# Optimization experiments

Hardware: AMD Instinct MI355X
Metric: run time of the kernel (lower is better)

## Reference

```python
import jax, jax.numpy as jnp
import numpy as np
from jax import lax

B, DIM, H, W = 4, 128, 128, 128
HEADS = 8
HID = int(DIM * 2.66)  # 340, IEL hidden_features
EPS_LN = 1e-6


def conv(x, w, b=None, groups=1, pad=0):
    out = lax.conv_general_dilated(
        x, w, (1, 1), [(pad, pad), (pad, pad)],
        feature_group_count=groups,
        dimension_numbers=('NCHW', 'OIHW', 'NCHW'))
    if b is not None:
        out = out + b[None, :, None, None]
    return out


def setup_inputs() -> dict:
    key = jax.random.key(0)
    ks = jax.random.split(key, 16)
    def wgt(k, shape, s=0.05):
        return jax.random.normal(k, shape, jnp.float32) * s
    return dict(
        x=jax.random.normal(ks[0], (B, DIM, H, W), jnp.float32),
        y=jax.random.normal(ks[1], (B, DIM, H, W), jnp.float32),
        ln_w=jnp.ones((DIM,), jnp.float32),
        ln_b=jnp.zeros((DIM,), jnp.float32),
        temperature=jnp.ones((HEADS, 1, 1), jnp.float32),
        q_w=wgt(ks[2], (DIM, DIM, 1, 1)),
        qdw_w=wgt(ks[3], (DIM, 1, 3, 3)),
        kv_w=wgt(ks[4], (2 * DIM, DIM, 1, 1)),
        kvdw_w=wgt(ks[5], (2 * DIM, 1, 3, 3)),
        po_w=wgt(ks[6], (DIM, DIM, 1, 1)),
        g1_w=wgt(ks[7], (DIM // 2, DIM, 1, 1)),
        g1_b=jnp.zeros((DIM // 2,), jnp.float32),
        g2_w=wgt(ks[8], (1, DIM // 2, 1, 1)),
        g2_b=jnp.zeros((1,), jnp.float32),
        pin_w=wgt(ks[9], (2 * HID, DIM, 1, 1)),
        dw_w=wgt(ks[10], (2 * HID, 1, 3, 3)),
        dw1_w=wgt(ks[11], (HID, 1, 3, 3)),
        dw2_w=wgt(ks[12], (HID, 1, 3, 3)),
        pout_w=wgt(ks[13], (DIM, HID, 1, 1)),
    )


def reference(x, y, ln_w, ln_b, temperature, q_w, qdw_w, kv_w, kvdw_w, po_w,
              g1_w, g1_b, g2_w, g2_b, pin_w, dw_w, dw1_w, dw2_w, pout_w):
    Bn, C, Hh, Ww = x.shape
    ch = C // HEADS  # channel tokens per head

    def ln(z):  # channels_first LayerNorm over channel axis
        u = z.mean(1, keepdims=True)
        s = ((z - u) ** 2).mean(1, keepdims=True)
        return ln_w[None, :, None, None] * ((z - u) / jnp.sqrt(s + EPS_LN)) + ln_b[None, :, None, None]

    xn = ln(x)
    yn = ln(y)

    # SCAB: transposed (channel) attention with dynamic top-k mask
    q = conv(conv(xn, q_w), qdw_w, groups=C, pad=1)
    kv = conv(conv(yn, kv_w), kvdw_w, groups=2 * C, pad=1)
    k, v = jnp.split(kv, 2, axis=1)
    q = q.reshape(Bn, HEADS, ch, Hh * Ww)
    k = k.reshape(Bn, HEADS, ch, Hh * Ww)
    v = v.reshape(Bn, HEADS, ch, Hh * Ww)
    q = q / jnp.maximum(jnp.linalg.norm(q, axis=-1, keepdims=True), 1e-12)
    k = k / jnp.maximum(jnp.linalg.norm(k, axis=-1, keepdims=True), 1e-12)

    # gate -> dynamic_k = int(ch * mean(gate)) as in torch (truncation)
    g = jax.nn.sigmoid(conv(jax.nn.relu(conv(xn, g1_w, g1_b)), g2_w, g2_b))
    dk = jnp.clip((ch * lax.stop_gradient(g).mean()).astype(jnp.int32), 1, ch)

    attn = jnp.einsum('bhcn,bhdn->bhcd', q, k) * temperature[None]  # [B,H,ch,ch]
    order = jnp.argsort(-attn, axis=-1)       # topk ordering (descending)
    ranks = jnp.argsort(order, axis=-1)       # rank of each entry in its row
    attn = jnp.where(ranks < dk, attn, -jnp.inf)
    attn = jax.nn.softmax(attn, axis=-1)
    out = jnp.einsum('bhcd,bhdn->bhcn', attn, v).reshape(Bn, C, Hh, Ww)
    x = x + conv(out, po_w)

    # IEL: tanh-gated dwconv FFN
    z = ln(x)
    t = conv(conv(z, pin_w), dw_w, groups=2 * HID, pad=1)
    x1, x2 = jnp.split(t, 2, axis=1)
    x1 = jnp.tanh(conv(x1, dw1_w, groups=HID, pad=1)) + x1
    x2 = jnp.tanh(conv(x2, dw2_w, groups=HID, pad=1)) + x2
    return conv(x1 * x2, pout_w) + x
```

## Files before the change

### kernel.cpp

```cpp
#include <hip/hip_runtime.h>
#include <math.h>

static constexpr int Bn    = 4;
static constexpr int Cc    = 128;
static constexpr int Hh    = 128;
static constexpr int Wb    = 128;
static constexpr int Nn    = Hh * Wb;
static constexpr int HEADS = 8;
static constexpr int CHh   = 16;
static constexpr int HID   = 340;
static constexpr int HID2  = 680;
static constexpr int NS    = 64;
static constexpr int MPAD  = 704;
static constexpr int KPAD2 = 352;

typedef unsigned short ushort_t;
typedef __attribute__((ext_vector_type(8))) short short8;
typedef __attribute__((ext_vector_type(4))) float f32x4;

__device__ __forceinline__ ushort_t f2bf(float f) {
    unsigned u = __float_as_uint(f);
    return (ushort_t)((u + 0x7FFFu + ((u >> 16) & 1u)) >> 16);
}
__device__ __forceinline__ float bf2f(ushort_t h) {
    return __uint_as_float(((unsigned)h) << 16);
}

__device__ __forceinline__ float fast_tanh(float x) {
    float a = fabsf(x);
    a = fminf(a, 12.0f);
    float e = __expf(2.0f * a);
    float r = 1.0f - 2.0f * __builtin_amdgcn_rcpf(e + 1.0f);
    return x < 0.0f ? -r : r;
}

__device__ __forceinline__ void iel_stage(float (*ts)[136], const ushort_t* __restrict__ tp,
                                          int gy0, int tid) {
    for (int idx = tid; idx < 640; idx += 256) {
        int i  = idx >> 5;
        int ch = idx & 31;
        int gy = gy0 - 2 + i;
        float v0, v1, v2, v3;
        if (gy >= 0 && gy < Hh) {
            uint2 u = *(const uint2*)(tp + gy * Wb + ch * 4);
            v0 = bf2f((ushort_t)(u.x & 0xFFFF)); v1 = bf2f((ushort_t)(u.x >> 16));
            v2 = bf2f((ushort_t)(u.y & 0xFFFF)); v3 = bf2f((ushort_t)(u.y >> 16));
        } else {
            v0 = v1 = v2 = v3 = 0.f;
        }
        float* dst = &ts[i][2 + ch * 4];
        float2 w0; w0.x = v0; w0.y = v1;
        float2 w1; w1.x = v2; w1.y = v3;
        *(float2*)dst       = w0;
        *(float2*)(dst + 2) = w1;
        if (ch == 0)  { ts[i][0]   = 0.f; ts[i][1]   = 0.f; }
        if (ch == 31) { ts[i][130] = 0.f; ts[i][131] = 0.f; }
    }
}

__global__ __launch_bounds__(256) void ln_kernel(const float* __restrict__ in,
                                                 const float* __restrict__ w,
                                                 const float* __restrict__ bias,
                                                 float* __restrict__ out) {
    int p = blockIdx.x * 256 + threadIdx.x;
    int b = blockIdx.z;
    const float* ib = in + (size_t)b * Cc * Nn + p;
    float s = 0.f, s2 = 0.f;
    #pragma unroll 8
    for (int c = 0; c < Cc; ++c) {
        float v = ib[(size_t)c * Nn];
        s += v; s2 += v * v;
    }
    float mean = s * (1.0f / Cc);
    float var  = s2 * (1.0f / Cc) - mean * mean;
    float inv  = 1.0f / sqrtf(var + 1e-6f);
    float* ob = out + (size_t)b * Cc * Nn + p;
    #pragma unroll 8
    for (int c = 0; c < Cc; ++c) {
        float v = ib[(size_t)c * Nn];
        ob[(size_t)c * Nn] = w[c] * ((v - mean) * inv) + bias[c];
    }
}

__global__ __launch_bounds__(256) void ln_bf16_kernel(const float* __restrict__ in,
                                                      const float* __restrict__ w,
                                                      const float* __restrict__ bias,
                                                      ushort_t* __restrict__ out) {
    int p = blockIdx.x * 256 + threadIdx.x;
    int b = blockIdx.z;
    const float* ib = in + (size_t)b * Cc * Nn + p;
    float s = 0.f, s2 = 0.f;
    #pragma unroll 8
    for (int c = 0; c < Cc; ++c) {
        float v = ib[(size_t)c * Nn];
        s += v; s2 += v * v;
    }
    float mean = s * (1.0f / Cc);
    float var  = s2 * (1.0f / Cc) - mean * mean;
    float inv  = 1.0f / sqrtf(var + 1e-6f);
    ushort_t* ob = out + (size_t)b * Cc * Nn + p;
    #pragma unroll 8
    for (int c = 0; c < Cc; ++c) {
        float v = ib[(size_t)c * Nn];
        ob[(size_t)c * Nn] = f2bf(w[c] * ((v - mean) * inv) + bias[c]);
    }
}

__global__ __launch_bounds__(256) void wconv_pad_rows_kernel(const float* __restrict__ w,
                                                             ushort_t* __restrict__ o,
                                                             int rows, int K) {
    int idx = blockIdx.x * 256 + threadIdx.x;
    int r = idx / K, k = idx - r * K;
    o[idx] = (r < rows) ? f2bf(w[(size_t)r * K + k]) : (ushort_t)0;
}
__global__ __launch_bounds__(256) void wconv_pad_cols_kernel(const float* __restrict__ w,
                                                             ushort_t* __restrict__ o,
                                                             int K, int Kp) {
    int idx = blockIdx.x * 256 + threadIdx.x;
    int r = idx / Kp, k = idx - r * Kp;
    o[idx] = (k < K) ? f2bf(w[(size_t)r * K + k]) : (ushort_t)0;
}

__global__ __launch_bounds__(256) void zero_f32_kernel(float* __restrict__ p, int n) {
    int i = blockIdx.x * 256 + threadIdx.x;
    if (i < n) p[i] = 0.f;
}

__global__ __launch_bounds__(256) void compose_w5_kernel(const float* __restrict__ dww,
                                                         const float* __restrict__ dw1p,
                                                         const float* __restrict__ dw2p,
                                                         float* __restrict__ w5) {
    int idx = blockIdx.x * 256 + threadIdx.x;
    if (idx >= 2 * HID * 25) return;
    int t   = idx / (HID * 25);
    int rem = idx - t * HID * 25;
    int c   = rem / 25;
    int e   = rem - c * 25;
    int dy  = e / 5, dx = e - dy * 5;
    const float* wa = dww + ((size_t)t * HID + c) * 9;
    const float* wb = (t ? dw2p : dw1p) + (size_t)c * 9;
    float acc = 0.f;
    #pragma unroll
    for (int a = 0; a < 3; ++a)
        #pragma unroll
        for (int b2 = 0; b2 < 3; ++b2) {
            int cy = dy - a, cx = dx - b2;
            if (cy >= 0 && cy < 3 && cx >= 0 && cx < 3)
                acc += wb[a * 3 + b2] * wa[cy * 3 + cx];
        }
    w5[idx] = acc;
}

__global__ __launch_bounds__(256) void gemm_bf16_kernel(const ushort_t* __restrict__ Zh,
                                                        const ushort_t* __restrict__ Wh,
                                                        const float* __restrict__ bias,
                                                        const float* __restrict__ res,
                                                        float* outf,
                                                        ushort_t* outh,
                                                        int Cin, int Kpad, int Mreal,
                                                        int act) {
    const int b    = blockIdx.z;
    const int px0  = blockIdx.x * 128;
    const int co0  = blockIdx.y * 64;
    const int tid  = threadIdx.x;
    const int wv   = tid >> 6;
    const int lane = tid & 63;
    const int n    = lane & 15;
    const int q    = lane >> 4;

    __shared__ ushort_t Bl[128][40];

    const ushort_t* Zb = Zh + (size_t)b * Cin * Nn;

    f32x4 acc[4][2];
    #pragma unroll
    for (int i = 0; i < 4; ++i)
        #pragma unroll
        for (int j = 0; j < 2; ++j) acc[i][j] = (f32x4){0.f, 0.f, 0.f, 0.f};

    for (int k0 = 0; k0 < Kpad; k0 += 32) {
        {
            int r = tid >> 3;
            int s = tid & 7;
            int ci = k0 + r;
            ushort_t tmp[16];
            if (ci < Cin) {
                const ushort_t* src = Zb + (size_t)ci * Nn + px0 + s * 16;
                uint4 v0 = *(const uint4*)src;
                uint4 v1 = *(const uint4*)(src + 8);
                tmp[0]  = (ushort_t)(v0.x & 0xFFFF); tmp[1]  = (ushort_t)(v0.x >> 16);
                tmp[2]  = (ushort_t)(v0.y & 0xFFFF); tmp[3]  = (ushort_t)(v0.y >> 16);
                tmp[4]  = (ushort_t)(v0.z & 0xFFFF); tmp[5]  = (ushort_t)(v0.z >> 16);
                tmp[6]  = (ushort_t)(v0.w & 0xFFFF); tmp[7]  = (ushort_t)(v0.w >> 16);
                tmp[8]  = (ushort_t)(v1.x & 0xFFFF); tmp[9]  = (ushort_t)(v1.x >> 16);
                tmp[10] = (ushort_t)(v1.y & 0xFFFF); tmp[11] = (ushort_t)(v1.y >> 16);
                tmp[12] = (ushort_t)(v1.z & 0xFFFF); tmp[13] = (ushort_t)(v1.z >> 16);
                tmp[14] = (ushort_t)(v1.w & 0xFFFF); tmp[15] = (ushort_t)(v1.w >> 16);
            } else {
                #pragma unroll
                for (int i = 0; i < 16; ++i) tmp[i] = 0;
            }
            #pragma unroll
            for (int i = 0; i < 16; ++i) Bl[s * 16 + i][r] = tmp[i];
        }
        __syncthreads();

        short8 bfrag[2];
        #pragma unroll
        for (int px16 = 0; px16 < 2; ++px16)
            bfrag[px16] = *(const short8*)&Bl[wv * 32 + px16 * 16 + n][q * 8];
        #pragma unroll
        for (int mt = 0; mt < 4; ++mt) {
            const ushort_t* wp = Wh + (size_t)(co0 + mt * 16 + n) * Kpad + k0 + q * 8;
            short8 afrag = *(const short8*)wp;
            #pragma unroll
            for (int px16 = 0; px16 < 2; ++px16)
                acc[mt][px16] = __builtin_amdgcn_mfma_f32_16x16x32_bf16(
                    afrag, bfrag[px16], acc[mt][px16], 0, 0, 0);
        }
        __syncthreads();
    }

    #pragma unroll
    for (int px16 = 0; px16 < 2; ++px16) {
        int px = px0 + wv * 32 + px16 * 16 + n;
        #pragma unroll
        for (int mt = 0; mt < 4; ++mt) {
            #pragma unroll
            for (int reg = 0; reg < 4; ++reg) {
                int co = co0 + mt * 16 + q * 4 + reg;
                if (co < Mreal) {
                    float v = acc[mt][px16][reg];
                    if (bias) v += bias[co];
                    if (act == 1) v = fmaxf(v, 0.f);
                    size_t o = ((size_t)b * Mreal + co) * Nn + px;
                    if (res)  v += res[o];
                    if (outf) outf[o] = v;
                    if (outh) outh[o] = f2bf(v);
                }
            }
        }
    }
}

template <int TCO>
__global__ __launch_bounds__(256) void conv1x1v_kernel(const float* __restrict__ in,
                                                       const float* __restrict__ wgt,
                                                       int wstride,
                                                       const float* __restrict__ bias,
                                                       const float* __restrict__ res,
                                                       float* __restrict__ out,
                                                       int Cin, int Cout, int act) {
    int pg  = blockIdx.x * 256 + threadIdx.x;
    int b   = blockIdx.z;
    int co0 = blockIdx.y * TCO;

    const float* wrow[TCO];
    #pragma unroll
    for (int i = 0; i < TCO; ++i) {
        int co = co0 + i; if (co > Cout - 1) co = Cout - 1;
        wrow[i] = wgt + (size_t)co * wstride;
    }

    float4 acc[TCO];
    #pragma unroll
    for (int i = 0; i < TCO; ++i) acc[i] = make_float4(0.f, 0.f, 0.f, 0.f);

    const float* ib = in + (size_t)b * Cin * Nn + (size_t)pg * 4;
    #pragma unroll 8
    for (int ci = 0; ci < Cin; ++ci) {
        float4 v = *(const float4*)(ib + (size_t)ci * Nn);
        #pragma unroll
        for (int i = 0; i < TCO; ++i) {
            float w = wrow[i][ci];
            acc[i].x += v.x * w; acc[i].y += v.y * w;
            acc[i].z += v.z * w; acc[i].w += v.w * w;
        }
    }

    #pragma unroll
    for (int i = 0; i < TCO; ++i) {
        int co = co0 + i;
        if (co < Cout) {
            float4 r = acc[i];
            if (bias) { float bb = bias[co]; r.x += bb; r.y += bb; r.z += bb; r.w += bb; }
            if (act == 1) {
                r.x = fmaxf(r.x, 0.f); r.y = fmaxf(r.y, 0.f);
                r.z = fmaxf(r.z, 0.f); r.w = fmaxf(r.w, 0.f);
            }
            size_t o = ((size_t)b * Cout + co) * Nn + (size_t)pg * 4;
            if (res) {
                float4 rv = *(const float4*)(res + o);
                r.x += rv.x; r.y += rv.y; r.z += rv.z; r.w += rv.w;
            }
            *(float4*)(out + o) = r;
        }
    }
}

__global__ __launch_bounds__(256) void dw3x3_kernel(const float* __restrict__ in,
                                                    const float* __restrict__ w,
                                                    float* __restrict__ out, int Ct) {
    int p = blockIdx.x * 256 + threadIdx.x;
    int c = blockIdx.y;
    int b = blockIdx.z;
    int y = p >> 7, x = p & (Wb - 1);
    const float* ib = in + ((size_t)b * Ct + c) * Nn;
    float wl[9];
    #pragma unroll
    for (int k = 0; k < 9; ++k) wl[k] = w[c * 9 + k];
    float acc = 0.f;
    #pragma unroll
    for (int dy = 0; dy < 3; ++dy) {
        int yy = y + dy - 1;
        if (yy < 0 || yy >= Hh) continue;
        #pragma unroll
        for (int dx = 0; dx < 3; ++dx) {
            int xx = x + dx - 1;
            if (xx < 0 || xx >= Wb) continue;
            acc += wl[dy * 3 + dx] * ib[yy * Wb + xx];
        }
    }
    out[((size_t)b * Ct + c) * Nn + p] = acc;
}

__global__ __launch_bounds__(256) void dw3x3_bf16_v2_kernel(const ushort_t* __restrict__ in,
                                                            const float* __restrict__ w,
                                                            float* __restrict__ out, int Ct,
                                                            float* __restrict__ ssq,
                                                            int nrmC) {
    const int gy0 = blockIdx.x * 16;
    const int c   = blockIdx.y;
    const int b   = blockIdx.z;
    const int tid = threadIdx.x;

    __shared__ float ts[20][136];

    const ushort_t* ib = in + ((size_t)b * Ct + c) * Nn;
    iel_stage(ts, ib, gy0, tid);
    __syncthreads();

    float wl[9];
    #pragma unroll
    for (int k = 0; k < 9; ++k) wl[k] = w[c * 9 + k];

    float* ob = out + ((size_t)b * Ct + c) * Nn;
    float s2sum = 0.f;
    #pragma unroll
    for (int it = 0; it < 2; ++it) {
        int idx = tid + it * 256;
        int r  = idx >> 5;
        int x0 = (idx & 31) * 4;
        float a[4] = {0.f, 0.f, 0.f, 0.f};
        #pragma unroll
        for (int dy = 0; dy < 3; ++dy) {
            const float* row = &ts[r + 1 + dy][x0];
            float4 va = *(const float4*)row;
            float4 vb = *(const float4*)(row + 4);
            float e[8] = {va.x, va.y, va.z, va.w, vb.x, vb.y, vb.z, vb.w};
            const float* wr = wl + dy * 3;
            #pragma unroll
            for (int p = 0; p < 4; ++p)
                a[p] += wr[0] * e[p + 1] + wr[1] * e[p + 2] + wr[2] * e[p + 3];
        }
        float4 st; st.x = a[0]; st.y = a[1]; st.z = a[2]; st.w = a[3];
        *(float4*)(ob + (gy0 + r) * Wb + x0) = st;
        s2sum += a[0] * a[0] + a[1] * a[1] + a[2] * a[2] + a[3] * a[3];
    }

    if (ssq != nullptr && c < nrmC) {
        #pragma unroll
        for (int o = 32; o > 0; o >>= 1) s2sum += __shfl_xor(s2sum, o, 64);
        if ((tid & 63) == 0) atomicAdd(&ssq[(size_t)b * nrmC + c], s2sum);
    }
}

__global__ __launch_bounds__(256) void l2norm_kernel(float* __restrict__ data, int cstride) {
    int b = blockIdx.z, c = blockIdx.x;
    float* ptr = data + ((size_t)b * cstride + c) * Nn;
    int t = threadIdx.x;
    float s = 0.f;
    for (int i = t; i < Nn; i += 256) { float v = ptr[i]; s += v * v; }
    __shared__ float red[256];
    red[t] = s; __syncthreads();
    for (int st = 128; st > 0; st >>= 1) { if (t < st) red[t] += red[t + st]; __syncthreads(); }
    float scale = 1.0f / fmaxf(sqrtf(red[0]), 1e-12f);
    for (int i = t; i < Nn; i += 256) ptr[i] *= scale;
}

__global__ __launch_bounds__(256) void gate2_kernel(const float* __restrict__ gmid,
                                                    const float* __restrict__ w2,
                                                    const float* __restrict__ b2,
                                                    float* __restrict__ blocksums,
                                                    int out_off) {
    int p = blockIdx.x * 256 + threadIdx.x;
    int b = blockIdx.z;
    float acc = b2[0];
    const float* ib = gmid + (size_t)b * 64 * Nn + p;
    #pragma unroll 8
    for (int ci = 0; ci < 64; ++ci) acc += ib[(size_t)ci * Nn] * w2[ci];
    float g = 1.0f / (1.0f + expf(-acc));
    __shared__ float red[256];
    int t = threadIdx.x;
    red[t] = g; __syncthreads();
    for (int st = 128; st > 0; st >>= 1) { if (t < st) red[t] += red[t + st]; __syncthreads(); }
    if (t == 0) blocksums[out_off + b * 64 + blockIdx.x] = red[0];
}

__global__ void gate_final_kernel(const float* __restrict__ blocksums,
                                  int* __restrict__ dk_out) {
    __shared__ double sred[256];
    int t = threadIdx.x;
    sred[t] = (double)blocksums[t];
    __syncthreads();
    for (int st = 128; st > 0; st >>= 1) { if (t < st) sred[t] += sred[t + st]; __syncthreads(); }
    if (t == 0) {
        double mean = sred[0] / (double)(Bn * Nn);
        float val = 16.0f * (float)mean;
        int dk = (int)val;
        if (dk < 1) dk = 1;
        if (dk > 16) dk = 16;
        *dk_out = dk;
    }
}

__global__ __launch_bounds__(256) void attn_qk_partial_kernel(const float* __restrict__ q,
                                                              const float* __restrict__ k,
                                                              int kstride,
                                                              float* __restrict__ partial) {
    int ns = blockIdx.x, h = blockIdx.y, b = blockIdx.z;
    int t = threadIdx.x;
    int c = t >> 4, d = t & 15;
    __shared__ float qs[16][65];
    __shared__ float ks[16][65];
    const float* qb = q + ((size_t)b * Cc + h * CHh) * Nn;
    const float* kb = k + ((size_t)b * kstride + h * CHh) * Nn;
    float acc = 0.f;
    int nbeg = ns * (Nn / NS);
    for (int n0 = nbeg; n0 < nbeg + (Nn / NS); n0 += 64) {
        for (int idx = t; idx < 1024; idx += 256) {
            int r = idx >> 6, col = idx & 63;
            qs[r][col] = qb[(size_t)r * Nn + n0 + col];
            ks[r][col] = kb[(size_t)r * Nn + n0 + col];
        }
        __syncthreads();
        #pragma unroll
        for (int j = 0; j < 64; ++j) acc += qs[c][j] * ks[d][j];
        __syncthreads();
    }
    partial[(((size_t)(b * HEADS + h)) * NS + ns) * 256 + t] = acc;
}

__global__ __launch_bounds__(256) void attn_reduce_kernel(const float* __restrict__ partial,
                                                          const float* __restrict__ temp,
                                                          const float* __restrict__ qss,
                                                          const float* __restrict__ kss,
                                                          float* __restrict__ attnp) {
    int bh = blockIdx.x;
    int h = bh % HEADS;
    int t = threadIdx.x;
    const float* pp = partial + (size_t)bh * NS * 256 + t;
    float s = 0.f;
    #pragma unroll 8
    for (int ns = 0; ns < NS; ++ns) s += pp[(size_t)ns * 256];
    float scale = temp[h];
    if (qss != nullptr) {
        int b  = bh / HEADS;
        int cQ = h * CHh + (t >> 4);
        int cK = h * CHh + (t & 15);
        float nq = fmaxf(sqrtf(qss[(size_t)b * Cc + cQ]), 1e-12f);
        float nk = fmaxf(sqrtf(kss[(size_t)b * Cc + cK]), 1e-12f);
        scale = scale / (nq * nk);
    }
    attnp[(size_t)bh * 256 + t] = s * scale;
}

__global__ void topk_softmax_kernel(float* __restrict__ attnp, const int* __restrict__ dkp) {
    int bh = blockIdx.x;
    int c = threadIdx.x;
    if (c >= 16) return;
    float* row = attnp + ((size_t)bh * CHh + c) * CHh;
    float a[16];
    #pragma unroll
    for (int d = 0; d < 16; ++d) a[d] = row[d];
    int dk = *dkp;
    unsigned keep = 0;
    float m = -INFINITY;
    #pragma unroll
    for (int d = 0; d < 16; ++d) {
        int rank = 0;
        #pragma unroll
        for (int j = 0; j < 16; ++j)
            rank += (a[j] > a[d]) || (a[j] == a[d] && j < d);
        if (rank < dk) { keep |= (1u << d); m = fmaxf(m, a[d]); }
    }
    float e[16]; float s = 0.f;
    #pragma unroll
    for (int d = 0; d < 16; ++d) {
        e[d] = (keep >> d & 1u) ? expf(a[d] - m) : 0.f;
        s += e[d];
    }
    float invs = 1.0f / s;
    #pragma unroll
    for (int d = 0; d < 16; ++d) row[d] = e[d] * invs;
}

__global__ __launch_bounds__(256) void attn_v_kernel(const float* __restrict__ attnp,
                                                     const float* __restrict__ v,
                                                     float* __restrict__ out) {
    int p = blockIdx.x * 256 + threadIdx.x;
    int cg = blockIdx.y;
    int b = blockIdx.z;
    int h = cg >> 4, cr = cg & 15;
    const float* arow = attnp + (((size_t)b * HEADS + h) * CHh + cr) * CHh;
    const float* vb = v + ((size_t)b * Cc + h * CHh) * Nn + p;
    float acc = 0.f;
    #pragma unroll
    for (int d = 0; d < 16; ++d) acc += arow[d] * vb[(size_t)d * Nn];
    out[((size_t)b * Cc + cg) * Nn + p] = acc;
}

__global__ __launch_bounds__(256) void attn_v_bf16_kernel(const float* __restrict__ attnp,
                                                          const float* __restrict__ v,
                                                          int vstride, int voff,
                                                          ushort_t* __restrict__ out) {
    int p = blockIdx.x * 256 + threadIdx.x;
    int cg = blockIdx.y;
    int b = blockIdx.z;
    int h = cg >> 4, cr = cg & 15;
    const float* arow = attnp + (((size_t)b * HEADS + h) * CHh + cr) * CHh;
    const float* vb = v + ((size_t)b * vstride + voff + h * CHh) * Nn + p;
    float acc = 0.f;
    #pragma unroll
    for (int d = 0; d < 16; ++d) acc += arow[d] * vb[(size_t)d * Nn];
    out[((size_t)b * Cc + cg) * Nn + p] = f2bf(acc);
}

__device__ __forceinline__ void iel_accum(const float (*ts)[136], int r, int x0,
                                          const float* __restrict__ w5,
                                          const float* __restrict__ wa,
                                          float a5[4], float a3[4]) {
    #pragma unroll
    for (int p = 0; p < 4; ++p) { a5[p] = 0.f; a3[p] = 0.f; }
    #pragma unroll
    for (int dy = 0; dy < 5; ++dy) {
        const float* row = &ts[r + dy][x0];
        float4 va = *(const float4*)row;
        float4 vb = *(const float4*)(row + 4);
        float e[8] = {va.x, va.y, va.z, va.w, vb.x, vb.y, vb.z, vb.w};
        const float* wr = w5 + dy * 5;
        #pragma unroll
        for (int p = 0; p < 4; ++p)
            a5[p] += wr[0] * e[p] + wr[1] * e[p + 1] + wr[2] * e[p + 2]
                   + wr[3] * e[p + 3] + wr[4] * e[p + 4];
        if (dy >= 1 && dy <= 3) {
            const float* wc = wa + (dy - 1) * 3;
            #pragma unroll
            for (int p = 0; p < 4; ++p)
                a3[p] += wc[0] * e[p + 1] + wc[1] * e[p + 2] + wc[2] * e[p + 3];
        }
    }
}

__global__ __launch_bounds__(256) void iel_tail_v5_kernel(const ushort_t* __restrict__ Th,
                                                          const float* __restrict__ dww,
                                                          const float* __restrict__ w5p,
                                                          ushort_t* __restrict__ PRh) {
    const int gy0 = blockIdx.x * 16;
    const int c   = blockIdx.y;
    const int b   = blockIdx.z;
    const int tid = threadIdx.x;

    __shared__ float ts[20][136];

    const ushort_t* t1 = Th + ((size_t)b * HID2 + c) * Nn;
    const ushort_t* t2 = Th + ((size_t)b * HID2 + HID + c) * Nn;
    ushort_t* outp = PRh + ((size_t)b * HID + c) * Nn;

    const float* w5g0 = w5p + (size_t)c * 25;
    const float* w5g1 = w5p + (size_t)(HID + c) * 25;
    const float* wag0 = dww + (size_t)c * 9;
    const float* wag1 = dww + (size_t)(HID + c) * 9;

    float keep[2][4];

    iel_stage(ts, t1, gy0, tid);
    __syncthreads();
    #pragma unroll
    for (int it = 0; it < 2; ++it) {
        int idx = tid + it * 256;
        int r  = idx >> 5;
        int x0 = (idx & 31) * 4;
        float a5[4], a3[4];
        iel_accum(ts, r, x0, w5g0, wag0, a5, a3);
        #pragma unroll
        for (int p = 0; p < 4; ++p) keep[it][p] = fast_tanh(a5[p]) + a3[p];
    }
    __syncthreads();

    iel_stage(ts, t2, gy0, tid);
    __syncthreads();
    #pragma unroll
    for (int it = 0; it < 2; ++it) {
        int idx = tid + it * 256;
        int r  = idx >> 5;
        int x0 = (idx & 31) * 4;
        float a5[4], a3[4];
        iel_accum(ts, r, x0, w5g1, wag1, a5, a3);
        float v0 = keep[it][0] * (fast_tanh(a5[0]) + a3[0]);
        float v1 = keep[it][1] * (fast_tanh(a5[1]) + a3[1]);
        float v2 = keep[it][2] * (fast_tanh(a5[2]) + a3[2]);
        float v3 = keep[it][3] * (fast_tanh(a5[3]) + a3[3]);
        uint2 pk;
        pk.x = (unsigned)f2bf(v0) | ((unsigned)f2bf(v1) << 16);
        pk.y = (unsigned)f2bf(v2) | ((unsigned)f2bf(v3) << 16);
        *(uint2*)(outp + (gy0 + r) * Wb + x0) = pk;
    }
}

__global__ __launch_bounds__(256) void iel_tail_f32_kernel(const float* __restrict__ t1p,
                                                           const float* __restrict__ t2p,
                                                           const float* __restrict__ dwA,
                                                           const float* __restrict__ dwB,
                                                           const float* __restrict__ dw1p,
                                                           const float* __restrict__ dw2p,
                                                           float* __restrict__ prod) {
    const int c = blockIdx.y;
    const int tilesx = Wb / 16;
    const int ty0 = (blockIdx.x / tilesx) * 16;
    const int tx0 = (blockIdx.x % tilesx) * 16;
    const int tid = threadIdx.x;

    __shared__ float ts[2][20][24];
    __shared__ float us[2][18][24];

    const float* t1 = t1p + (size_t)c * Nn;
    const float* t2 = t2p + (size_t)c * Nn;

    for (int idx = tid; idx < 400; idx += 256) {
        int i = idx / 20, j = idx % 20;
        int gy = ty0 - 2 + i, gx = tx0 - 2 + j;
        bool ok = (gy >= 0 && gy < Hh && gx >= 0 && gx < Wb);
        ts[0][i][j] = ok ? t1[gy * Wb + gx] : 0.f;
        ts[1][i][j] = ok ? t2[gy * Wb + gx] : 0.f;
    }
    __syncthreads();

    float wA[9], wB[9], w1[9], w2[9];
    #pragma unroll
    for (int k = 0; k < 9; ++k) {
        wA[k] = dwA[c * 9 + k];
        wB[k] = dwB[c * 9 + k];
        w1[k] = dw1p[c * 9 + k];
        w2[k] = dw2p[c * 9 + k];
    }

    for (int idx = tid; idx < 324; idx += 256) {
        int i = idx / 18, j = idx % 18;
        int gy = ty0 - 1 + i, gx = tx0 - 1 + j;
        float a0 = 0.f, a1 = 0.f;
        if (gy >= 0 && gy < Hh && gx >= 0 && gx < Wb) {
            #pragma unroll
            for (int dy = 0; dy < 3; ++dy)
                #pragma unroll
                for (int dx = 0; dx < 3; ++dx) {
                    a0 += wA[dy * 3 + dx] * ts[0][i + dy][j + dx];
                    a1 += wB[dy * 3 + dx] * ts[1][i + dy][j + dx];
                }
        }
        us[0][i][j] = a0;
        us[1][i][j] = a1;
    }
    __syncthreads();

    int ty = tid >> 4, tx = tid & 15;
    float c1 = us[0][ty + 1][tx + 1];
    float c2 = us[1][ty + 1][tx + 1];
    float s1 = 0.f, s2 = 0.f;
    #pragma unroll
    for (int dy = 0; dy < 3; ++dy)
        #pragma unroll
        for (int dx = 0; dx < 3; ++dx) {
            s1 += w1[dy * 3 + dx] * us[0][ty + dy][tx + dx];
            s2 += w2[dy * 3 + dx] * us[1][ty + dy][tx + dx];
        }
    float x1t = tanhf(s1) + c1;
    float x2t = tanhf(s2) + c2;
    prod[(size_t)c * Nn + (ty0 + ty) * Wb + (tx0 + tx)] = x1t * x2t;
}

extern "C" void kernel_launch(void* const* d_in, const int* in_sizes, int n_in,
                              void* d_out, int out_size, void* d_ws, size_t ws_size,
                              hipStream_t stream) {
    const float* x      = (const float*)d_in[0];
    const float* y      = (const float*)d_in[1];
    const float* ln_w   = (const float*)d_in[2];
    const float* ln_b   = (const float*)d_in[3];
    const float* temp   = (const float*)d_in[4];
    const float* q_w    = (const float*)d_in[5];
    const float* qdw_w  = (const float*)d_in[6];
    const float* kv_w   = (const float*)d_in[7];
    const float* kvdw_w = (const float*)d_in[8];
    const float* po_w   = (const float*)d_in[9];
    const float* g1_w   = (const float*)d_in[10];
    const float* g1_b   = (const float*)d_in[11];
    const float* g2_w   = (const float*)d_in[12];
    const float* g2_b   = (const float*)d_in[13];
    const float* pin_w  = (const float*)d_in[14];
    const float* dw_w   = (const float*)d_in[15];
    const float* dw1_w  = (const float*)d_in[16];
    const float* dw2_w  = (const float*)d_in[17];
    const float* pout_w = (const float*)d_in[18];
    float* out = (float*)d_out;

    char* ws = (char*)d_ws;
    float* attn      = (float*)ws;
    float* blocksums = (float*)(ws + 32768);
    int*   dk        = (int*)(ws + 33792);
    ushort_t* qWh  = (ushort_t*)(ws + 34816);
    ushort_t* kvWh = qWh + 16384;
    ushort_t* poWh = kvWh + 32768;
    ushort_t* g1Wh = poWh + 16384;
    ushort_t* Wh1  = g1Wh + 8192;
    ushort_t* Wh2  = Wh1 + (size_t)MPAD * Cc;
    float* qss = (float*)(ws + 458752);
    float* kss = (float*)(ws + 460800);
    float* w5  = (float*)(ws + 462848);
    float* pool    = (float*)(ws + (1u << 20));

    const size_t CN    = (size_t)Cc * Nn;
    const size_t SLOT1 = (size_t)Bn * CN;
    const size_t TIER1_NEED = 65536 + 6 * SLOT1 * 4;

    dim3 blk(256);
    const int PGX = Nn / 1024;

    if (ws_size >= TIER1_NEED) {
        float* S3 = pool;
        float* S4 = pool + 8 * 1024 * 1024;
        ushort_t* XNh  = (ushort_t*)(pool + 24 * 1024 * 1024);
        ushort_t* YNh  = XNh + Bn * CN;
        ushort_t* KV1h = YNh + Bn * CN;
        ushort_t* Q1h  = KV1h + 2 * Bn * CN;
        float* gmid    = (float*)Q1h;
        float* partial = gmid;
        ushort_t* AOh  = XNh;

        wconv_pad_rows_kernel<<<dim3(64), blk, 0, stream>>>(q_w, qWh, 128, Cc);
        wconv_pad_rows_kernel<<<dim3(128), blk, 0, stream>>>(kv_w, kvWh, 256, Cc);
        wconv_pad_rows_kernel<<<dim3(64), blk, 0, stream>>>(po_w, poWh, 128, Cc);
        wconv_pad_rows_kernel<<<dim3(32), blk, 0, stream>>>(g1_w, g1Wh, 64, Cc);
        wconv_pad_rows_kernel<<<dim3(MPAD * Cc / 256), blk, 0, stream>>>(pin_w, Wh1, HID2, Cc);
        wconv_pad_cols_kernel<<<dim3(Cc * KPAD2 / 256), blk, 0, stream>>>(pout_w, Wh2, HID, KPAD2);
        zero_f32_kernel<<<dim3(4), blk, 0, stream>>>(qss, 2 * Bn * Cc);
        compose_w5_kernel<<<dim3((2 * HID * 25 + 255) / 256), blk, 0, stream>>>(
            dw_w, dw1_w, dw2_w, w5);

        ln_bf16_kernel<<<dim3(Nn / 256, 1, Bn), blk, 0, stream>>>(x, ln_w, ln_b, XNh);
        ln_bf16_kernel<<<dim3(Nn / 256, 1, Bn), blk, 0, stream>>>(y, ln_w, ln_b, YNh);

        gemm_bf16_kernel<<<dim3(Nn / 128, 2, Bn), blk, 0, stream>>>(
            XNh, qWh, nullptr, nullptr, nullptr, Q1h, Cc, Cc, Cc, 0);
        dw3x3_bf16_v2_kernel<<<dim3(Hh / 16, Cc, Bn), blk, 0, stream>>>(
            Q1h, qdw_w, S3, Cc, qss, Cc);

        gemm_bf16_kernel<<<dim3(Nn / 128, 4, Bn), blk, 0, stream>>>(
            YNh, kvWh, nullptr, nullptr, nullptr, KV1h, Cc, Cc, 2 * Cc, 0);
        dw3x3_bf16_v2_kernel<<<dim3(Hh / 16, 2 * Cc, Bn), blk, 0, stream>>>(
            KV1h, kvdw_w, S4, 2 * Cc, kss, Cc);

        gemm_bf16_kernel<<<dim3(Nn / 128, 1, Bn), blk, 0, stream>>>(
            XNh, g1Wh, g1_b, nullptr, gmid, nullptr, Cc, Cc, 64, 1);
        gate2_kernel<<<dim3(Nn / 256, 1, Bn), blk, 0, stream>>>(gmid, g2_w, g2_b, blocksums, 0);
        gate_final_kernel<<<dim3(1), blk, 0, stream>>>(blocksums, dk);

        attn_qk_partial_kernel<<<dim3(NS, HEADS, Bn), blk, 0, stream>>>(S3, S4, 2 * Cc, partial);
        attn_reduce_kernel<<<dim3(Bn * HEADS), blk, 0, stream>>>(partial, temp, qss, kss, attn);
        topk_softmax_kernel<<<dim3(Bn * HEADS), dim3(16), 0, stream>>>(attn, dk);
        attn_v_bf16_kernel<<<dim3(Nn / 256, Cc, Bn), blk, 0, stream>>>(
            attn, S4, 2 * Cc, Cc, AOh);

        gemm_bf16_kernel<<<dim3(Nn / 128, 2, Bn), blk, 0, stream>>>(
            AOh, poWh, nullptr, x, out, nullptr, Cc, Cc, Cc, 0);

        ushort_t* ZNh = (ushort_t*)pool;
        ushort_t* Th  = ZNh + Bn * CN;
        ushort_t* PRh = Th + (size_t)Bn * HID2 * Nn;

        ln_bf16_kernel<<<dim3(Nn / 256, 1, Bn), blk, 0, stream>>>(out, ln_w, ln_b, ZNh);

        gemm_bf16_kernel<<<dim3(Nn / 128, MPAD / 64, Bn), blk, 0, stream>>>(
            ZNh, Wh1, nullptr, nullptr, nullptr, Th, Cc, Cc, HID2, 0);

        iel_tail_v5_kernel<<<dim3(Hh / 16, HID, Bn), blk, 0, stream>>>(
            Th, dw_w, w5, PRh);

        gemm_bf16_kernel<<<dim3(Nn / 128, 2, Bn), blk, 0, stream>>>(
            PRh, Wh2, nullptr, out, out, nullptr, HID, KPAD2, Cc, 0);
    } else {
        float* s0 = pool;
        float* s1 = pool + 1 * CN;
        float* s2 = pool + 2 * CN;
        float* s3 = pool + 3 * CN;
        float* s4 = pool + 4 * CN;
        float* s5 = pool + 5 * CN;

        for (int b = 0; b < Bn; ++b) {
            const float* xb = x + (size_t)b * CN;
            ln_kernel<<<dim3(Nn / 256, 1, 1), blk, 0, stream>>>(xb, ln_w, ln_b, s0);
            conv1x1v_kernel<4><<<dim3(PGX, 16, 1), blk, 0, stream>>>(
                s0, g1_w, Cc, g1_b, nullptr, s1, Cc, 64, 1);
            gate2_kernel<<<dim3(Nn / 256, 1, 1), blk, 0, stream>>>(
                s1, g2_w, g2_b, blocksums, b * 64);
        }
        gate_final_kernel<<<dim3(1), blk, 0, stream>>>(blocksums, dk);

        for (int b = 0; b < Bn; ++b) {
            const float* xb = x + (size_t)b * CN;
            const float* yb = y + (size_t)b * CN;
            float* outb = out + (size_t)b * CN;
            float* attnb = attn + (size_t)b * HEADS * CHh * CHh;

            ln_kernel<<<dim3(Nn / 256, 1, 1), blk, 0, stream>>>(xb, ln_w, ln_b, s0);
            ln_kernel<<<dim3(Nn / 256, 1, 1), blk, 0, stream>>>(yb, ln_w, ln_b, s1);

            conv1x1v_kernel<8><<<dim3(PGX, 16, 1), blk, 0, stream>>>(
                s0, q_w, Cc, nullptr, nullptr, s2, Cc, Cc, 0);
            dw3x3_kernel<<<dim3(Nn / 256, Cc, 1), blk, 0, stream>>>(s2, qdw_w, s3, Cc);
            l2norm_kernel<<<dim3(Cc, 1, 1), blk, 0, stream>>>(s3, Cc);

            conv1x1v_kernel<8><<<dim3(PGX, 16, 1), blk, 0, stream>>>(
                s1, kv_w, Cc, nullptr, nullptr, s2, Cc, Cc, 0);
            dw3x3_kernel<<<dim3(Nn / 256, Cc, 1), blk, 0, stream>>>(s2, kvdw_w, s4, Cc);
            l2norm_kernel<<<dim3(Cc, 1, 1), blk, 0, stream>>>(s4, Cc);

            conv1x1v_kernel<8><<<dim3(PGX, 16, 1), blk, 0, stream>>>(
                s1, kv_w + 128 * 128, Cc, nullptr, nullptr, s2, Cc, Cc, 0);
            dw3x3_kernel<<<dim3(Nn / 256, Cc, 1), blk, 0, stream>>>(s2, kvdw_w + 128 * 9, s5, Cc);

            attn_qk_partial_kernel<<<dim3(NS, HEADS, 1), blk, 0, stream>>>(s3, s4, Cc, s2);
            attn_reduce_kernel<<<dim3(HEADS), blk, 0, stream>>>(s2, temp, nullptr, nullptr, attnb);
            topk_softmax_kernel<<<dim3(HEADS), dim3(16), 0, stream>>>(attnb, dk);
            attn_v_kernel<<<dim3(Nn / 256, Cc, 1), blk, 0, stream>>>(attnb, s5, s2);

            conv1x1v_kernel<8><<<dim3(PGX, 16, 1), blk, 0, stream>>>(
                s2, po_w, Cc, nullptr, xb, outb, Cc, Cc, 0);
        }

        const int CHUNK = 170;
        const size_t TCH = (size_t)CHUNK * Nn;
        float* zn   = pool;
        float* T1   = pool + CN;
        float* T2   = T1 + TCH;
        float* prod = T2 + TCH;
        for (int b = 0; b < Bn; ++b) {
            float* outb = out + (size_t)b * CN;
            ln_kernel<<<dim3(Nn / 256, 1, 1), blk, 0, stream>>>(outb, ln_w, ln_b, zn);
            for (int c0 = 0; c0 < HID; c0 += CHUNK) {
                conv1x1v_kernel<20><<<dim3(PGX, 9, 1), blk, 0, stream>>>(
                    zn, pin_w + (size_t)c0 * Cc, Cc, nullptr, nullptr, T1, Cc, CHUNK, 0);
                conv1x1v_kernel<20><<<dim3(PGX, 9, 1), blk, 0, stream>>>(
                    zn, pin_w + (size_t)(HID + c0) * Cc, Cc, nullptr, nullptr, T2, Cc, CHUNK, 0);
                iel_tail_f32_kernel<<<dim3(64, CHUNK, 1), blk, 0, stream>>>(
                    T1, T2, dw_w + c0 * 9, dw_w + (HID + c0) * 9,
                    dw1_w + c0 * 9, dw2_w + c0 * 9, prod);
                conv1x1v_kernel<8><<<dim3(PGX, 16, 1), blk, 0, stream>>>(
                    prod, pout_w + c0, HID, nullptr, outb, outb, CHUNK, Cc, 0);
            }
        }
    }
}
```

Measured before the change: 641.5 us.

## Replace composed 5x5 IEL conv with two-stage 3x3 via shared-memory intermediate

```diff
diff --git a/kernel.cpp b/kernel.cpp
--- a/kernel.cpp
+++ b/kernel.cpp
@@ -34,28 +34,96 @@
     return x < 0.0f ? -r : r;
 }
 
-__device__ __forceinline__ void iel_stage(float (*ts)[136], const ushort_t* __restrict__ tp,
-                                          int gy0, int tid) {
-    for (int idx = tid; idx < 640; idx += 256) {
-        int i  = idx >> 5;
-        int ch = idx & 31;
+__device__ __forceinline__ void iel6_stage(float (*ts)[144], const ushort_t* __restrict__ tp,
+                                           int gy0, int tid) {
+    for (int idx = tid; idx < 360; idx += 256) {
+        int i = idx / 18;
+        int j = idx - i * 18;
         int gy = gy0 - 2 + i;
-        float v0, v1, v2, v3;
+        float v[8];
+        if (j >= 1 && j <= 16 && gy >= 0 && gy < Hh) {
+            uint4 u = *(const uint4*)(tp + gy * Wb + (j - 1) * 8);
+            v[0] = bf2f((ushort_t)(u.x & 0xFFFF)); v[1] = bf2f((ushort_t)(u.x >> 16));
+            v[2] = bf2f((ushort_t)(u.y & 0xFFFF)); v[3] = bf2f((ushort_t)(u.y >> 16));
+            v[4] = bf2f((ushort_t)(u.z & 0xFFFF)); v[5] = bf2f((ushort_t)(u.z >> 16));
+            v[6] = bf2f((ushort_t)(u.w & 0xFFFF)); v[7] = bf2f((ushort_t)(u.w >> 16));
+        } else {
+            #pragma unroll
+            for (int k = 0; k < 8; ++k) v[k] = 0.f;
+        }
+        float4 a; a.x = v[0]; a.y = v[1]; a.z = v[2]; a.w = v[3];
+        float4 bq; bq.x = v[4]; bq.y = v[5]; bq.z = v[6]; bq.w = v[7];
+        *(float4*)&ts[i][8 * j]     = a;
+        *(float4*)&ts[i][8 * j + 4] = bq;
+    }
+}
+
+__device__ __forceinline__ void iel6_ustage(const float (*ts)[144], float (*us)[144],
+                                            const float* __restrict__ wa9,
+                                            int gy0, int tid) {
+    float wa[9];
+    #pragma unroll
+    for (int k = 0; k < 9; ++k) wa[k] = wa9[k];
+    for (int idx = tid; idx < 306; idx += 256) {
+        int i = idx / 17;
+        int k = idx - i * 17;
+        int gy = gy0 - 1 + i;
+        float a[8] = {0.f, 0.f, 0.f, 0.f, 0.f, 0.f, 0.f, 0.f};
         if (gy >= 0 && gy < Hh) {
-            uint2 u = *(const uint2*)(tp + gy * Wb + ch * 4);
-            v0 = bf2f((ushort_t)(u.x & 0xFFFF)); v1 = bf2f((ushort_t)(u.x >> 16));
-            v2 = bf2f((ushort_t)(u.y & 0xFFFF)); v3 = bf2f((ushort_t)(u.y >> 16));
-        } else {
-            v0 = v1 = v2 = v3 = 0.f;
-        }
-        float* dst = &ts[i][2 + ch * 4];
-        float2 w0; w0.x = v0; w0.y = v1;
-        float2 w1; w1.x = v2; w1.y = v3;
-        *(float2*)dst       = w0;
-        *(float2*)(dst + 2) = w1;
-        if (ch == 0)  { ts[i][0]   = 0.f; ts[i][1]   = 0.f; }
-        if (ch == 31) { ts[i][130] = 0.f; ts[i][131] = 0.f; }
-    }
+            #pragma unroll
+            for (int dy = 0; dy < 3; ++dy) {
+                const float* row = &ts[i + dy][8 * k];
+                float4 e0 = *(const float4*)row;
+                float4 e1 = *(const float4*)(row + 4);
+                float4 e2 = *(const float4*)(row + 8);
+                float e[12] = {e0.x, e0.y, e0.z, e0.w, e1.x, e1.y, e1.z, e1.w,
+                               e2.x, e2.y, e2.z, e2.w};
+                float w0 = wa[dy * 3], w1 = wa[dy * 3 + 1], w2 = wa[dy * 3 + 2];
+                #pragma unroll
+                for (int p = 0; p < 8; ++p)
+                    a[p] += w0 * e[p + 2] + w1 * e[p + 3] + w2 * e[p + 4];
+            }
+            #pragma unroll
+            for (int p = 0; p < 8; ++p) {
+                int gx = 8 * k - 5 + p;
+                if (gx < 0 || gx > 127) a[p] = 0.f;
+            }
+        }
+        float4 o0; o0.x = a[0]; o0.y = a[1]; o0.z = a[2]; o0.w = a[3];
+        float4 o1; o1.x = a[4]; o1.y = a[5]; o1.z = a[6]; o1.w = a[7];
+        *(float4*)&us[i][8 * k]     = o0;
+        *(float4*)&us[i][8 * k + 4] = o1;
+    }
+}
+
+__device__ __forceinline__ void iel6_outer(const float (*us)[144],
+                                           const float* __restrict__ wb9,
+                                           int r, int s, float res[8]) {
+    float wb[9];
+    #pragma unroll
+    for (int k = 0; k < 9; ++k) wb[k] = wb9[k];
+    int x0 = 8 * s;
+    float aa[8] = {0.f, 0.f, 0.f, 0.f, 0.f, 0.f, 0.f, 0.f};
+    float ctr[8];
+    #pragma unroll
+    for (int dy = 0; dy < 3; ++dy) {
+        const float* row = &us[r + dy][x0 + 4];
+        float4 e0 = *(const float4*)row;
+        float4 e1 = *(const float4*)(row + 4);
+        float4 e2 = *(const float4*)(row + 8);
+        float e[12] = {e0.x, e0.y, e0.z, e0.w, e1.x, e1.y, e1.z, e1.w,
+                       e2.x, e2.y, e2.z, e2.w};
+        float w0 = wb[dy * 3], w1 = wb[dy * 3 + 1], w2 = wb[dy * 3 + 2];
+        #pragma unroll
+        for (int p = 0; p < 8; ++p)
+            aa[p] += w0 * e[p] + w1 * e[p + 1] + w2 * e[p + 2];
+        if (dy == 1) {
+            #pragma unroll
+            for (int p = 0; p < 8; ++p) ctr[p] = e[p + 1];
+        }
+    }
+    #pragma unroll
+    for (int p = 0; p < 8; ++p) res[p] = fast_tanh(aa[p]) + ctr[p];
 }
 
 __global__ __launch_bounds__(256) void ln_kernel(const float* __restrict__ in,
@@ -124,31 +192,6 @@
 __global__ __launch_bounds__(256) void zero_f32_kernel(float* __restrict__ p, int n) {
     int i = blockIdx.x * 256 + threadIdx.x;
     if (i < n) p[i] = 0.f;
-}
-
-__global__ __launch_bounds__(256) void compose_w5_kernel(const float* __restrict__ dww,
-                                                         const float* __restrict__ dw1p,
-                                                         const float* __restrict__ dw2p,
-                                                         float* __restrict__ w5) {
-    int idx = blockIdx.x * 256 + threadIdx.x;
-    if (idx >= 2 * HID * 25) return;
-    int t   = idx / (HID * 25);
-    int rem = idx - t * HID * 25;
-    int c   = rem / 25;
-    int e   = rem - c * 25;
-    int dy  = e / 5, dx = e - dy * 5;
-    const float* wa = dww + ((size_t)t * HID + c) * 9;
-    const float* wb = (t ? dw2p : dw1p) + (size_t)c * 9;
-    float acc = 0.f;
-    #pragma unroll
-    for (int a = 0; a < 3; ++a)
-        #pragma unroll
-        for (int b2 = 0; b2 < 3; ++b2) {
-            int cy = dy - a, cx = dx - b2;
-            if (cy >= 0 && cy < 3 && cx >= 0 && cx < 3)
-                acc += wb[a * 3 + b2] * wa[cy * 3 + cx];
-        }
-    w5[idx] = acc;
 }
 
 __global__ __launch_bounds__(256) void gemm_bf16_kernel(const ushort_t* __restrict__ Zh,
@@ -334,41 +377,44 @@
     const int b   = blockIdx.z;
     const int tid = threadIdx.x;
 
-    __shared__ float ts[20][136];
+    __shared__ float ts[20][144];
 
     const ushort_t* ib = in + ((size_t)b * Ct + c) * Nn;
-    iel_stage(ts, ib, gy0, tid);
+    iel6_stage(ts, ib, gy0, tid);
     __syncthreads();
 
     float wl[9];
     #pragma unroll
     for (int k = 0; k < 9; ++k) wl[k] = w[c * 9 + k];
 
-    float* ob = out + ((size_t)b * Ct + c) * Nn;
-    float s2sum = 0.f;
-    #pragma unroll
-    for (int it = 0; it < 2; ++it) {
-        int idx = tid + it * 256;
-        int r  = idx >> 5;
-        int x0 = (idx & 31) * 4;
-        float a[4] = {0.f, 0.f, 0.f, 0.f};
-        #pragma unroll
-        for (int dy = 0; dy < 3; ++dy) {
-            const float* row = &ts[r + 1 + dy][x0];
-            float4 va = *(const float4*)row;
-            float4 vb = *(const float4*)(row + 4);
-            float e[8] = {va.x, va.y, va.z, va.w, vb.x, vb.y, vb.z, vb.w};
-            const float* wr = wl + dy * 3;
-            #pragma unroll
-            for (int p = 0; p < 4; ++p)
-                a[p] += wr[0] * e[p + 1] + wr[1] * e[p + 2] + wr[2] * e[p + 3];
-        }
-        float4 st; st.x = a[0]; st.y = a[1]; st.z = a[2]; st.w = a[3];
-        *(float4*)(ob + (gy0 + r) * Wb + x0) = st;
-        s2sum += a[0] * a[0] + a[1] * a[1] + a[2] * a[2] + a[3] * a[3];
-    }
+    const int r = tid >> 4;
+    const int s = tid & 15;
+    int x0 = 8 * s;
+    float a[8] = {0.f, 0.f, 0.f, 0.f, 0.f, 0.f, 0.f, 0.f};
+    #pragma unroll
+    for (int dy = 0; dy < 3; ++dy) {
+        const float* row = &ts[r + 1 + dy][x0 + 4];
+        float4 e0 = *(const float4*)row;
+        float4 e1 = *(const float4*)(row + 4);
+        float4 e2 = *(const float4*)(row + 8);
+        float4 e3 = *(const float4*)(row + 12);
+        float e[16] = {e0.x, e0.y, e0.z, e0.w, e1.x, e1.y, e1.z, e1.w,
+                       e2.x, e2.y, e2.z, e2.w, e3.x, e3.y, e3.z, e3.w};
+        float w0 = wl[dy * 3], w1 = wl[dy * 3 + 1], w2 = wl[dy * 3 + 2];
+        #pragma unroll
+        for (int p = 0; p < 8; ++p)
+            a[p] += w0 * e[p + 3] + w1 * e[p + 4] + w2 * e[p + 5];
+    }
+    float* ob = out + ((size_t)b * Ct + c) * Nn + (gy0 + r) * Wb + x0;
+    float4 s0; s0.x = a[0]; s0.y = a[1]; s0.z = a[2]; s0.w = a[3];
+    float4 s1; s1.x = a[4]; s1.y = a[5]; s1.z = a[6]; s1.w = a[7];
+    *(float4*)ob       = s0;
+    *(float4*)(ob + 4) = s1;
 
     if (ssq != nullptr && c < nrmC) {
+        float s2sum = 0.f;
+        #pragma unroll
+        for (int p = 0; p < 8; ++p) s2sum += a[p] * a[p];
         #pragma unroll
         for (int o = 32; o > 0; o >>= 1) s2sum += __shfl_xor(s2sum, o, 64);
         if ((tid & 63) == 0) atomicAdd(&ssq[(size_t)b * nrmC + c], s2sum);
@@ -536,86 +582,43 @@
     out[((size_t)b * Cc + cg) * Nn + p] = f2bf(acc);
 }
 
-__device__ __forceinline__ void iel_accum(const float (*ts)[136], int r, int x0,
-                                          const float* __restrict__ w5,
-                                          const float* __restrict__ wa,
-                                          float a5[4], float a3[4]) {
-    #pragma unroll
-    for (int p = 0; p < 4; ++p) { a5[p] = 0.f; a3[p] = 0.f; }
-    #pragma unroll
-    for (int dy = 0; dy < 5; ++dy) {
-        const float* row = &ts[r + dy][x0];
-        float4 va = *(const float4*)row;
-        float4 vb = *(const float4*)(row + 4);
-        float e[8] = {va.x, va.y, va.z, va.w, vb.x, vb.y, vb.z, vb.w};
-        const float* wr = w5 + dy * 5;
-        #pragma unroll
-        for (int p = 0; p < 4; ++p)
-            a5[p] += wr[0] * e[p] + wr[1] * e[p + 1] + wr[2] * e[p + 2]
-                   + wr[3] * e[p + 3] + wr[4] * e[p + 4];
-        if (dy >= 1 && dy <= 3) {
-            const float* wc = wa + (dy - 1) * 3;
-            #pragma unroll
-            for (int p = 0; p < 4; ++p)
-                a3[p] += wc[0] * e[p + 1] + wc[1] * e[p + 2] + wc[2] * e[p + 3];
-        }
-    }
-}
-
-__global__ __launch_bounds__(256) void iel_tail_v5_kernel(const ushort_t* __restrict__ Th,
+__global__ __launch_bounds__(256) void iel_tail_v6_kernel(const ushort_t* __restrict__ Th,
                                                           const float* __restrict__ dww,
-                                                          const float* __restrict__ w5p,
+                                                          const float* __restrict__ dw1p,
+                                                          const float* __restrict__ dw2p,
                                                           ushort_t* __restrict__ PRh) {
     const int gy0 = blockIdx.x * 16;
     const int c   = blockIdx.y;
     const int b   = blockIdx.z;
     const int tid = threadIdx.x;
-
-    __shared__ float ts[20][136];
+    const int r   = tid >> 4;
+    const int s   = tid & 15;
+
+    __shared__ float ts[20][144];
+    __shared__ float us[18][144];
 
     const ushort_t* t1 = Th + ((size_t)b * HID2 + c) * Nn;
     const ushort_t* t2 = Th + ((size_t)b * HID2 + HID + c) * Nn;
     ushort_t* outp = PRh + ((size_t)b * HID + c) * Nn;
 
-    const float* w5g0 = w5p + (size_t)c * 25;
-    const float* w5g1 = w5p + (size_t)(HID + c) * 25;
-    const float* wag0 = dww + (size_t)c * 9;
-    const float* wag1 = dww + (size_t)(HID + c) * 9;
-
-    float keep[2][4];
-
-    iel_stage(ts, t1, gy0, tid);
+    iel6_stage(ts, t1, gy0, tid);
     __syncthreads();
-    #pragma unroll
-    for (int it = 0; it < 2; ++it) {
-        int idx = tid + it * 256;
-        int r  = idx >> 5;
-        int x0 = (idx & 31) * 4;
-        float a5[4], a3[4];
-        iel_accum(ts, r, x0, w5g0, wag0, a5, a3);
-        #pragma unroll
-        for (int p = 0; p < 4; ++p) keep[it][p] = fast_tanh(a5[p]) + a3[p];
-    }
+    iel6_ustage(ts, us, dww + (size_t)c * 9, gy0, tid);
     __syncthreads();
-
-    iel_stage(ts, t2, gy0, tid);
+    iel6_stage(ts, t2, gy0, tid);
+    float keep[8];
+    iel6_outer(us, dw1p + (size_t)c * 9, r, s, keep);
     __syncthreads();
-    #pragma unroll
-    for (int it = 0; it < 2; ++it) {
-        int idx = tid + it * 256;
-        int r  = idx >> 5;
-        int x0 = (idx & 31) * 4;
-        float a5[4], a3[4];
-        iel_accum(ts, r, x0, w5g1, wag1, a5, a3);
-        float v0 = keep[it][0] * (fast_tanh(a5[0]) + a3[0]);
-        float v1 = keep[it][1] * (fast_tanh(a5[1]) + a3[1]);
-        float v2 = keep[it][2] * (fast_tanh(a5[2]) + a3[2]);
-        float v3 = keep[it][3] * (fast_tanh(a5[3]) + a3[3]);
-        uint2 pk;
-        pk.x = (unsigned)f2bf(v0) | ((unsigned)f2bf(v1) << 16);
-        pk.y = (unsigned)f2bf(v2) | ((unsigned)f2bf(v3) << 16);
-        *(uint2*)(outp + (gy0 + r) * Wb + x0) = pk;
-    }
+    iel6_ustage(ts, us, dww + (size_t)(HID + c) * 9, gy0, tid);
+    __syncthreads();
+    float res[8];
+    iel6_outer(us, dw2p + (size_t)c * 9, r, s, res);
+    uint4 pk;
+    pk.x = (unsigned)f2bf(keep[0] * res[0]) | ((unsigned)f2bf(keep[1] * res[1]) << 16);
+    pk.y = (unsigned)f2bf(keep[2] * res[2]) | ((unsigned)f2bf(keep[3] * res[3]) << 16);
+    pk.z = (unsigned)f2bf(keep[4] * res[4]) | ((unsigned)f2bf(keep[5] * res[5]) << 16);
+    pk.w = (unsigned)f2bf(keep[6] * res[6]) | ((unsigned)f2bf(keep[7] * res[7]) << 16);
+    *(uint4*)(outp + (gy0 + r) * Wb + s * 8) = pk;
 }
 
 __global__ __launch_bounds__(256) void iel_tail_f32_kernel(const float* __restrict__ t1p,
@@ -725,7 +728,6 @@
     ushort_t* Wh2  = Wh1 + (size_t)MPAD * Cc;
     float* qss = (float*)(ws + 458752);
     float* kss = (float*)(ws + 460800);
-    float* w5  = (float*)(ws + 462848);
     float* pool    = (float*)(ws + (1u << 20));
 
     const size_t CN    = (size_t)Cc * Nn;
@@ -753,8 +755,6 @@
         wconv_pad_rows_kernel<<<dim3(MPAD * Cc / 256), blk, 0, stream>>>(pin_w, Wh1, HID2, Cc);
         wconv_pad_cols_kernel<<<dim3(Cc * KPAD2 / 256), blk, 0, stream>>>(pout_w, Wh2, HID, KPAD2);
         zero_f32_kernel<<<dim3(4), blk, 0, stream>>>(qss, 2 * Bn * Cc);
-        compose_w5_kernel<<<dim3((2 * HID * 25 + 255) / 256), blk, 0, stream>>>(
-            dw_w, dw1_w, dw2_w, w5);
 
         ln_bf16_kernel<<<dim3(Nn / 256, 1, Bn), blk, 0, stream>>>(x, ln_w, ln_b, XNh);
         ln_bf16_kernel<<<dim3(Nn / 256, 1, Bn), blk, 0, stream>>>(y, ln_w, ln_b, YNh);
@@ -792,8 +792,8 @@
         gemm_bf16_kernel<<<dim3(Nn / 128, MPAD / 64, Bn), blk, 0, stream>>>(
             ZNh, Wh1, nullptr, nullptr, nullptr, Th, Cc, Cc, HID2, 0);
 
-        iel_tail_v5_kernel<<<dim3(Hh / 16, HID, Bn), blk, 0, stream>>>(
-            Th, dw_w, w5, PRh);
+        iel_tail_v6_kernel<<<dim3(Hh / 16, HID, Bn), blk, 0, stream>>>(
+            Th, dw_w, dw1_w, dw2_w, PRh);
 
         gemm_bf16_kernel<<<dim3(Nn / 128, 2, Bn), blk, 0, stream>>>(
             PRh, Wh2, nullptr, out, out, nullptr, HID, KPAD2, Cc, 0);
```

Measured after the change: 661.5 us. 1.03x slower.
